# Kernel optimization log

Measured on AMD Instinct MI355X. Metric: run time of the kernel, lower is better.

Reference implementation:

```python
import jax, jax.numpy as jnp
import numpy as np

EPS = 1e-6
CONV_P = 3.0
GM_P = 2.0
NUM_NODES = 50000
NUM_EDGES = 600000
NUM_GRAPHS = 512
IN_DIM = 128
HID = 128
OUT_DIM = 64


def _scatter_mean(vals, index, num_segments):
    # scatter_mean with empty segments -> 0 (count clamped to 1)
    s = jax.ops.segment_sum(vals, index, num_segments=num_segments)
    cnt = jax.ops.segment_sum(jnp.ones((vals.shape[0],), vals.dtype), index,
                              num_segments=num_segments)
    return s / jnp.maximum(cnt, 1.0)[:, None]


def _signed_pow(v, p):
    return jnp.sign(v) * (jnp.abs(v) + EPS) ** p


def _spm_conv(x, W, b, src, dst, p):
    h = x @ W.T + b                      # [N, hid] linear
    msg = h[src]                          # gather x_j  [E, hid]
    t = _signed_pow(msg, p)
    pooled = _scatter_mean(t, dst, NUM_NODES)
    return _signed_pow(pooled, 1.0 / p)


def setup_inputs() -> dict:
    key = jax.random.key(0)
    ks = jax.random.split(key, 8)
    x = jax.random.normal(ks[0], (NUM_NODES, IN_DIM), jnp.float32)
    edge_index = jax.random.randint(ks[1], (2, NUM_EDGES), 0, NUM_NODES)
    batch = jnp.sort(jax.random.randint(ks[2], (NUM_NODES,), 0, NUM_GRAPHS))
    s1 = 1.0 / np.sqrt(IN_DIM)
    s2 = 1.0 / np.sqrt(HID)
    W1 = jax.random.uniform(ks[3], (HID, IN_DIM), jnp.float32, -s1, s1)
    b1 = jax.random.uniform(ks[4], (HID,), jnp.float32, -s1, s1)
    W2 = jax.random.uniform(ks[5], (HID, HID), jnp.float32, -s2, s2)
    b2 = jax.random.uniform(ks[6], (HID,), jnp.float32, -s2, s2)
    # final layer: orthogonal-init frozen weight (out_dim=64, hid=128)
    A = jax.random.normal(ks[7], (HID, OUT_DIM), jnp.float32)
    Q, _ = jnp.linalg.qr(A)
    Wout = Q.T                            # [OUT_DIM, HID], orthonormal rows
    bout = jax.random.uniform(jax.random.fold_in(key, 9), (OUT_DIM,),
                              jnp.float32, -s2, s2)
    return {"x": x, "W1": W1, "b1": b1, "W2": W2, "b2": b2,
            "Wout": Wout, "bout": bout, "edge_index": edge_index,
            "batch": batch}


def reference(x, W1, b1, W2, b2, Wout, bout, edge_index, batch):
    src, dst = edge_index[0], edge_index[1]
    h = _spm_conv(x, W1, b1, src, dst, CONV_P)
    h = jax.nn.relu(h)                    # relu between conv layers only
    h = _spm_conv(h, W2, b2, src, dst, CONV_P)
    # global generalized mean pool (signed)
    t = _signed_pow(h, GM_P)
    pooled = _scatter_mean(t, batch, NUM_GRAPHS)
    graph_repr = _signed_pow(pooled, 1.0 / GM_P)   # [G, HID]
    return graph_repr @ Wout.T + bout              # [G, OUT_DIM]
```

## Files before the change

### kernel.cpp

```cpp
#include <hip/hip_runtime.h>
#include <hip/hip_bf16.h>
#include <math.h>

#define N_NODES 50000
#define N_EDGES 600000
#define N_GRAPHS 512
#define DIM 128
#define OUTD 64
#define EPSV 1e-6f
#define BSTRIDE 64
#define EBLK4 586
#define PREP_BLK 64

typedef __attribute__((ext_vector_type(8))) short bf16x8;
typedef __attribute__((ext_vector_type(4))) float f32x4;

__device__ __forceinline__ float sgn(float v) {
    return (v > 0.f) ? 1.f : ((v < 0.f) ? -1.f : 0.f);
}

__device__ __forceinline__ float cube_signed(float v) {
    float m = fabsf(v) + EPSV;
    return sgn(v) * m * m * m;
}

__device__ __forceinline__ float cbrt_pos(float m) {
    return exp2f(log2f(m) * (1.0f / 3.0f));
}

__device__ __forceinline__ unsigned short f2bf(float f) {
    unsigned u = __float_as_uint(f);
    unsigned r = (u + 0x7fff + ((u >> 16) & 1)) >> 16;
    return (unsigned short)r;
}

__device__ __forceinline__ float bf2f(unsigned short h) {
    return __uint_as_float(((unsigned)h) << 16);
}

__device__ __forceinline__ void gather_acc8(const unsigned* __restrict__ T32,
                                            const unsigned short* __restrict__ bucket,
                                            int cnt, int lane, float2 acc[4]) {
    #pragma unroll
    for (int j = 0; j < 4; j++) acc[j] = make_float2(0.f, 0.f);
    if (cnt <= 0) return;
    int myidx = (lane < cnt) ? (int)bucket[lane] : 0;
    int sub = lane & 15, grp = lane >> 4;
    int cnt16 = (cnt + 15) & ~15;
    for (int i = 0; i < cnt16; i += 16) {
        uint4 u[4];
        #pragma unroll
        for (int c = 0; c < 4; c++) {
            int s = __shfl(myidx, i + c * 4 + grp, 64);
            u[c] = *(const uint4*)(T32 + (size_t)s * 64 + sub * 4);
        }
        #pragma unroll
        for (int c = 0; c < 4; c++) {
            acc[0].x += __uint_as_float(u[c].x << 16);
            acc[0].y += __uint_as_float(u[c].x & 0xffff0000u);
            acc[1].x += __uint_as_float(u[c].y << 16);
            acc[1].y += __uint_as_float(u[c].y & 0xffff0000u);
            acc[2].x += __uint_as_float(u[c].z << 16);
            acc[2].y += __uint_as_float(u[c].z & 0xffff0000u);
            acc[3].x += __uint_as_float(u[c].w << 16);
            acc[3].y += __uint_as_float(u[c].w & 0xffff0000u);
        }
    }
    #pragma unroll
    for (int j = 0; j < 4; j++) {
        acc[j].x += __shfl_xor(acc[j].x, 16, 64);
        acc[j].y += __shfl_xor(acc[j].y, 16, 64);
        acc[j].x += __shfl_xor(acc[j].x, 32, 64);
        acc[j].y += __shfl_xor(acc[j].y, 32, 64);
    }
}

__device__ __forceinline__ float acc_pick_x(const float2 acc[4], int grp) {
    return grp == 0 ? acc[0].x : grp == 1 ? acc[1].x : grp == 2 ? acc[2].x : acc[3].x;
}
__device__ __forceinline__ float acc_pick_y(const float2 acc[4], int grp) {
    return grp == 0 ? acc[0].y : grp == 1 ? acc[1].y : grp == 2 ? acc[2].y : acc[3].y;
}


__global__ void buildprep(const int* __restrict__ src, const int* __restrict__ dst,
                          int* __restrict__ deg, unsigned short* __restrict__ csr,
                          const float* __restrict__ W1, const float* __restrict__ W2,
                          unsigned short* __restrict__ W1hi, unsigned short* __restrict__ W1lo,
                          unsigned short* __restrict__ W2hi, unsigned short* __restrict__ W2lo,
                          const int* __restrict__ batch, int* __restrict__ gstart,
                          unsigned* __restrict__ T1z, unsigned* __restrict__ T2z) {
    int b = blockIdx.x;
    if (b < EBLK4) {
        int e4 = b * 256 + threadIdx.x;
        if (e4 < N_EDGES / 4) {
            uint4 s4 = ((const uint4*)src)[e4];
            uint4 d4 = ((const uint4*)dst)[e4];
            int d0 = (int)d4.x, d1 = (int)d4.y, d2 = (int)d4.z, d3 = (int)d4.w;
            int sl0 = atomicAdd(&deg[d0], 1);
            int sl1 = atomicAdd(&deg[d1], 1);
            int sl2 = atomicAdd(&deg[d2], 1);
            int sl3 = atomicAdd(&deg[d3], 1);
            if (sl0 < BSTRIDE) csr[d0 * BSTRIDE + sl0] = (unsigned short)(s4.x + 1);
            if (sl1 < BSTRIDE) csr[d1 * BSTRIDE + sl1] = (unsigned short)(s4.y + 1);
            if (sl2 < BSTRIDE) csr[d2 * BSTRIDE + sl2] = (unsigned short)(s4.z + 1);
            if (sl3 < BSTRIDE) csr[d3 * BSTRIDE + sl3] = (unsigned short)(s4.w + 1);
        }
        return;
    }
    int i = (b - EBLK4) * 256 + threadIdx.x;
    {
        float w = W1[i];
        unsigned short h = f2bf(w);
        W1hi[i] = h;
        W1lo[i] = f2bf(w - bf2f(h));
        w = W2[i];
        h = f2bf(w);
        W2hi[i] = h;
        W2lo[i] = f2bf(w - bf2f(h));
    }
    if (i < 64) { T1z[i] = 0u; T2z[i] = 0u; }
    if (i <= N_GRAPHS) {
        int lo = 0, hi = N_NODES;
        while (lo < hi) {
            int mid = (lo + hi) >> 1;
            if (batch[mid] < i) lo = mid + 1; else hi = mid;
        }
        gstart[i] = lo;
    }
}


__global__ __launch_bounds__(256) void linear_cube_mfma(const float* __restrict__ X,
                                                        const unsigned short* __restrict__ Whi,
                                                        const unsigned short* __restrict__ Wlo,
                                                        const float* __restrict__ B,
                                                        unsigned short* __restrict__ T) {
    __shared__ unsigned short Tl[4][16][DIM];
    int wave = threadIdx.x >> 6;
    int lane = threadIdx.x & 63;
    int tile = blockIdx.x * 4 + wave;
    if (tile >= N_NODES / 16) return;
    int n0 = tile * 16;
    int r = lane & 15;
    int g = lane >> 4;

    bf16x8 xh[4], xl[4];
    const float* xrow = X + (size_t)(n0 + r) * DIM + g * 8;
    #pragma unroll
    for (int kb = 0; kb < 4; kb++) {
        float4 a = *(const float4*)(xrow + kb * 32);
        float4 b = *(const float4*)(xrow + kb * 32 + 4);
        float v[8] = {a.x, a.y, a.z, a.w, b.x, b.y, b.z, b.w};
        #pragma unroll
        for (int j = 0; j < 8; j++) {
            unsigned short h = f2bf(v[j]);
            float rem = v[j] - bf2f(h);
            xh[kb][j] = (short)h;
            xl[kb][j] = (short)f2bf(rem);
        }
    }

    #pragma unroll
    for (int ct = 0; ct < 8; ct++) {
        const unsigned short* whbase = Whi + (size_t)(ct * 16 + r) * DIM + g * 8;
        const unsigned short* wlbase = Wlo + (size_t)(ct * 16 + r) * DIM + g * 8;
        f32x4 acc = {0.f, 0.f, 0.f, 0.f};
        #pragma unroll
        for (int kb = 0; kb < 4; kb++) {
            bf16x8 wh = *(const bf16x8*)(whbase + kb * 32);
            bf16x8 wl = *(const bf16x8*)(wlbase + kb * 32);
            acc = __builtin_amdgcn_mfma_f32_16x16x32_bf16(xh[kb], wh, acc, 0, 0, 0);
            acc = __builtin_amdgcn_mfma_f32_16x16x32_bf16(xl[kb], wh, acc, 0, 0, 0);
            acc = __builtin_amdgcn_mfma_f32_16x16x32_bf16(xh[kb], wl, acc, 0, 0, 0);
        }
        float bias = B[ct * 16 + r];
        #pragma unroll
        for (int q = 0; q < 4; q++) {
            int node = g * 4 + q;
            float h = acc[q] + bias;
            Tl[wave][node][ct * 16 + r] = f2bf(cube_signed(h));
        }
    }

    uint4* dstg = (uint4*)(T + (size_t)(n0 + 1) * DIM);
    const uint4* srcl = (const uint4*)&Tl[wave][0][0];
    #pragma unroll
    for (int i = 0; i < 4; i++) {
        dstg[i * 64 + lane] = srcl[i * 64 + lane];
    }
}


__global__ __launch_bounds__(512) void agg_linear_cube(const unsigned* __restrict__ T32,
                                                       const int* __restrict__ deg,
                                                       const unsigned short* __restrict__ csr,
                                                       const unsigned short* __restrict__ Whi,
                                                       const unsigned short* __restrict__ Wlo,
                                                       const float* __restrict__ B,
                                                       unsigned short* __restrict__ Tout) {
    __shared__ __attribute__((aligned(16))) unsigned Phi[16][68];
    __shared__ __attribute__((aligned(16))) unsigned Plo[16][68];
    int wave = threadIdx.x >> 6;
    int lane = threadIdx.x & 63;
    int n0 = blockIdx.x * 16;
    int sub = lane & 15, grp = lane >> 4;

    #pragma unroll
    for (int q = 0; q < 2; q++) {
        int row = wave * 2 + q;
        int nd = n0 + row;
        int d = deg[nd];
        int cnt = d < BSTRIDE ? d : BSTRIDE;
        float2 acc[4];
        gather_acc8(T32, csr + (size_t)nd * BSTRIDE, cnt, lane, acc);
        float c = (float)(d > 1 ? d : 1);
        float m0 = acc_pick_x(acc, grp) / c;
        float m1 = acc_pick_y(acc, grp) / c;
        float r0 = fmaxf(sgn(m0) * cbrt_pos(fabsf(m0) + EPSV), 0.f);
        float r1 = fmaxf(sgn(m1) * cbrt_pos(fabsf(m1) + EPSV), 0.f);
        unsigned short h0 = f2bf(r0), h1 = f2bf(r1);
        unsigned short l0 = f2bf(r0 - bf2f(h0)), l1 = f2bf(r1 - bf2f(h1));
        Phi[row][sub * 4 + grp] = (unsigned)h0 | ((unsigned)h1 << 16);
        Plo[row][sub * 4 + grp] = (unsigned)l0 | ((unsigned)l1 << 16);
    }
    __syncthreads();

    int r = lane & 15;
    int g = lane >> 4;
    bf16x8 xh[4], xl[4];
    #pragma unroll
    for (int kb = 0; kb < 4; kb++) {
        xh[kb] = *(const bf16x8*)&Phi[r][kb * 16 + g * 4];
        xl[kb] = *(const bf16x8*)&Plo[r][kb * 16 + g * 4];
    }
    int ct = wave;
    const unsigned short* whbase = Whi + (size_t)(ct * 16 + r) * DIM + g * 8;
    const unsigned short* wlbase = Wlo + (size_t)(ct * 16 + r) * DIM + g * 8;
    f32x4 acc = {0.f, 0.f, 0.f, 0.f};
    #pragma unroll
    for (int kb = 0; kb < 4; kb++) {
        bf16x8 wh = *(const bf16x8*)(whbase + kb * 32);
        bf16x8 wl = *(const bf16x8*)(wlbase + kb * 32);
        acc = __builtin_amdgcn_mfma_f32_16x16x32_bf16(xh[kb], wh, acc, 0, 0, 0);
        acc = __builtin_amdgcn_mfma_f32_16x16x32_bf16(xl[kb], wh, acc, 0, 0, 0);
        acc = __builtin_amdgcn_mfma_f32_16x16x32_bf16(xh[kb], wl, acc, 0, 0, 0);
    }
    float bias = B[ct * 16 + r];
    #pragma unroll
    for (int q = 0; q < 4; q++) {
        int node = g * 4 + q;
        float h = acc[q] + bias;
        Tout[(size_t)(n0 + node + 1) * DIM + ct * 16 + r] = f2bf(cube_signed(h));
    }
}


__global__ __launch_bounds__(256) void aggregate(const unsigned* __restrict__ T32,
                                                 const int* __restrict__ deg,
                                                 const unsigned short* __restrict__ csr,
                                                 float* __restrict__ P) {
    int nd = blockIdx.x * 4 + (threadIdx.x >> 6);
    if (nd >= N_NODES) return;
    int lane = threadIdx.x & 63;
    int sub = lane & 15, grp = lane >> 4;
    int d = deg[nd];
    int cnt = d < BSTRIDE ? d : BSTRIDE;
    float2 acc[4];
    gather_acc8(T32, csr + (size_t)nd * BSTRIDE, cnt, lane, acc);
    float c = (float)(d > 1 ? d : 1);
    float m0 = acc_pick_x(acc, grp) / c;
    float m1 = acc_pick_y(acc, grp) / c;
    float r0 = sgn(m0) * cbrt_pos(fabsf(m0) + EPSV);
    float r1 = sgn(m1) * cbrt_pos(fabsf(m1) + EPSV);
    *(float2*)(P + (size_t)nd * DIM + sub * 8 + grp * 2) = make_float2(r0, r1);
}


__global__ __launch_bounds__(128) void pool_final(const float* __restrict__ P,
                                                  const int* __restrict__ gstart,
                                                  const float* __restrict__ Wout,
                                                  const float* __restrict__ bout,
                                                  float* __restrict__ out) {
    __shared__ float R[DIM];
    __shared__ float partial[128];
    int g = blockIdx.x, f = threadIdx.x;
    int s = gstart[g], e = gstart[g + 1];
    float acc = 0.f;
    for (int i = s; i < e; i++) {
        float v = P[(size_t)i * DIM + f];
        float m = fabsf(v) + EPSV;
        acc += sgn(v) * m * m;
    }
    int cnt = e - s;
    float c = (float)(cnt > 1 ? cnt : 1);
    float mean = acc / c;
    R[f] = sgn(mean) * sqrtf(fabsf(mean) + EPSV);
    __syncthreads();

    int o = f & 63;
    int half = f >> 6;
    const float4* W4 = (const float4*)Wout + o * 32 + half * 16;
    const float4* R4 = (const float4*)R + half * 16;
    float a = 0.f;
    #pragma unroll
    for (int k = 0; k < 16; k++) {
        float4 w = W4[k];
        float4 r = R4[k];
        a += r.x * w.x + r.y * w.y + r.z * w.z + r.w * w.w;
    }
    partial[f] = a;
    __syncthreads();
    if (f < OUTD) out[(size_t)g * OUTD + f] = bout[f] + partial[f] + partial[f + 64];
}


extern "C" void kernel_launch(void* const* d_in, const int* in_sizes, int n_in,
                              void* d_out, int out_size, void* d_ws, size_t ws_size,
                              hipStream_t stream) {
    const float* x    = (const float*)d_in[0];
    const float* W1   = (const float*)d_in[1];
    const float* b1   = (const float*)d_in[2];
    const float* W2   = (const float*)d_in[3];
    const float* b2   = (const float*)d_in[4];
    const float* Wout = (const float*)d_in[5];
    const float* bout = (const float*)d_in[6];
    const int* edge   = (const int*)d_in[7];
    const int* batch  = (const int*)d_in[8];
    const int* srcp = edge;
    const int* dstp = edge + N_EDGES;
    float* out = (float*)d_out;

    char* ws = (char*)d_ws;
    size_t off = 0;
    auto alloc = [&](size_t bytes) -> char* {
        char* p = ws + off;
        off += (bytes + 255) / 256 * 256;
        return p;
    };
    unsigned short* T1 = (unsigned short*)alloc((size_t)(N_NODES + 1) * DIM * 2);
    unsigned short* T2 = (unsigned short*)alloc((size_t)(N_NODES + 1) * DIM * 2);
    float* P        = (float*)alloc((size_t)N_NODES * DIM * 4);
    int*   deg      = (int*)alloc((size_t)N_NODES * 4);
    unsigned short* csr = (unsigned short*)alloc((size_t)N_NODES * BSTRIDE * 2);
    int*   gstart   = (int*)alloc((size_t)(N_GRAPHS + 1) * 4);
    unsigned short* W1hi = (unsigned short*)alloc((size_t)DIM * DIM * 2);
    unsigned short* W1lo = (unsigned short*)alloc((size_t)DIM * DIM * 2);
    unsigned short* W2hi = (unsigned short*)alloc((size_t)DIM * DIM * 2);
    unsigned short* W2lo = (unsigned short*)alloc((size_t)DIM * DIM * 2);

    hipMemsetAsync(deg, 0, (size_t)N_NODES * 4, stream);
    buildprep<<<EBLK4 + PREP_BLK, 256, 0, stream>>>(srcp, dstp, deg, csr,
                                                    W1, W2, W1hi, W1lo, W2hi, W2lo,
                                                    batch, gstart,
                                                    (unsigned*)T1, (unsigned*)T2);

    const int TILES = N_NODES / 16;
    const int LBLK = (TILES + 3) / 4;
    const int ABLK = (N_NODES + 3) / 4;
    linear_cube_mfma<<<LBLK, 256, 0, stream>>>(x, W1hi, W1lo, b1, T1);
    agg_linear_cube<<<TILES, 512, 0, stream>>>((const unsigned*)T1, deg, csr,
                                               W2hi, W2lo, b2, T2);
    aggregate<<<ABLK, 256, 0, stream>>>((const unsigned*)T2, deg, csr, P);
    pool_final<<<N_GRAPHS, 128, 0, stream>>>(P, gstart, Wout, bout, out);
}
```

Baseline: 182.9 us.

## Split neighbor aggregation into feature-sliced passes and unfuse second linear layer

Replaces the fused aggregate+linear kernel and the separate aggregate kernel with one feature-sliced gather kernel run in four passes over 32-column slices. Each pass touches one quarter of the node feature table, so the gathered working set is more likely to stay in L2 cache across random neighbor accesses. The second linear layer becomes a standalone MFMA kernel reading hi/lo bf16 splits from global buffers. This costs four times the index loads and shuffles, extra global round-trips for the intermediate, and an added launch.

Result: slower. 388.7 us (+112.6%).

```diff
diff --git a/kernel.cpp b/kernel.cpp
--- a/kernel.cpp
+++ b/kernel.cpp
@@ -11,9 +11,11 @@
 #define BSTRIDE 64
 #define EBLK4 586
 #define PREP_BLK 64
+#define NGRP 12500
 
 typedef __attribute__((ext_vector_type(8))) short bf16x8;
 typedef __attribute__((ext_vector_type(4))) float f32x4;
+typedef __attribute__((ext_vector_type(4))) unsigned u32x4;
 
 __device__ __forceinline__ float sgn(float v) {
     return (v > 0.f) ? 1.f : ((v < 0.f) ? -1.f : 0.f);
@@ -36,50 +38,6 @@
 
 __device__ __forceinline__ float bf2f(unsigned short h) {
     return __uint_as_float(((unsigned)h) << 16);
-}
-
-__device__ __forceinline__ void gather_acc8(const unsigned* __restrict__ T32,
-                                            const unsigned short* __restrict__ bucket,
-                                            int cnt, int lane, float2 acc[4]) {
-    #pragma unroll
-    for (int j = 0; j < 4; j++) acc[j] = make_float2(0.f, 0.f);
-    if (cnt <= 0) return;
-    int myidx = (lane < cnt) ? (int)bucket[lane] : 0;
-    int sub = lane & 15, grp = lane >> 4;
-    int cnt16 = (cnt + 15) & ~15;
-    for (int i = 0; i < cnt16; i += 16) {
-        uint4 u[4];
-        #pragma unroll
-        for (int c = 0; c < 4; c++) {
-            int s = __shfl(myidx, i + c * 4 + grp, 64);
-            u[c] = *(const uint4*)(T32 + (size_t)s * 64 + sub * 4);
-        }
-        #pragma unroll
-        for (int c = 0; c < 4; c++) {
-            acc[0].x += __uint_as_float(u[c].x << 16);
-            acc[0].y += __uint_as_float(u[c].x & 0xffff0000u);
-            acc[1].x += __uint_as_float(u[c].y << 16);
-            acc[1].y += __uint_as_float(u[c].y & 0xffff0000u);
-            acc[2].x += __uint_as_float(u[c].z << 16);
-            acc[2].y += __uint_as_float(u[c].z & 0xffff0000u);
-            acc[3].x += __uint_as_float(u[c].w << 16);
-            acc[3].y += __uint_as_float(u[c].w & 0xffff0000u);
-        }
-    }
-    #pragma unroll
-    for (int j = 0; j < 4; j++) {
-        acc[j].x += __shfl_xor(acc[j].x, 16, 64);
-        acc[j].y += __shfl_xor(acc[j].y, 16, 64);
-        acc[j].x += __shfl_xor(acc[j].x, 32, 64);
-        acc[j].y += __shfl_xor(acc[j].y, 32, 64);
-    }
-}
-
-__device__ __forceinline__ float acc_pick_x(const float2 acc[4], int grp) {
-    return grp == 0 ? acc[0].x : grp == 1 ? acc[1].x : grp == 2 ? acc[2].x : acc[3].x;
-}
-__device__ __forceinline__ float acc_pick_y(const float2 acc[4], int grp) {
-    return grp == 0 ? acc[0].y : grp == 1 ? acc[1].y : grp == 2 ? acc[2].y : acc[3].y;
 }
 
 
@@ -192,88 +150,136 @@
 }
 
 
-__global__ __launch_bounds__(512) void agg_linear_cube(const unsigned* __restrict__ T32,
-                                                       const int* __restrict__ deg,
-                                                       const unsigned short* __restrict__ csr,
-                                                       const unsigned short* __restrict__ Whi,
-                                                       const unsigned short* __restrict__ Wlo,
-                                                       const float* __restrict__ B,
-                                                       unsigned short* __restrict__ Tout) {
-    __shared__ __attribute__((aligned(16))) unsigned Phi[16][68];
-    __shared__ __attribute__((aligned(16))) unsigned Plo[16][68];
+__global__ __launch_bounds__(256) void agg_sliced(const unsigned* __restrict__ T32,
+                                                  const int* __restrict__ deg,
+                                                  const unsigned short* __restrict__ csr,
+                                                  unsigned* __restrict__ Phi,
+                                                  unsigned* __restrict__ Plo,
+                                                  float* __restrict__ P, int mode) {
+    int bid = blockIdx.x;
+    int pass = bid / NGRP;
+    int grp = bid - pass * NGRP;
     int wave = threadIdx.x >> 6;
     int lane = threadIdx.x & 63;
-    int n0 = blockIdx.x * 16;
-    int sub = lane & 15, grp = lane >> 4;
-
-    #pragma unroll
-    for (int q = 0; q < 2; q++) {
-        int row = wave * 2 + q;
-        int nd = n0 + row;
-        int d = deg[nd];
-        int cnt = d < BSTRIDE ? d : BSTRIDE;
-        float2 acc[4];
-        gather_acc8(T32, csr + (size_t)nd * BSTRIDE, cnt, lane, acc);
+    int nd = grp * 4 + wave;
+    int es = lane >> 2, q = lane & 3;
+
+    int d = deg[nd];
+    int cnt = d < BSTRIDE ? d : BSTRIDE;
+    const unsigned short* bucket = csr + (size_t)nd * BSTRIDE;
+    int myidx = (lane < cnt) ? (int)__builtin_nontemporal_load(&bucket[lane]) : 0;
+
+    float a[8];
+    #pragma unroll
+    for (int j = 0; j < 8; j++) a[j] = 0.f;
+
+    for (int i = 0; i < cnt; i += 16) {
+        int s = __shfl(myidx, i + es, 64);
+        u32x4 u = *(const u32x4*)(T32 + (size_t)s * 64 + pass * 16 + q * 4);
+        a[0] += __uint_as_float(u.x << 16);
+        a[1] += __uint_as_float(u.x & 0xffff0000u);
+        a[2] += __uint_as_float(u.y << 16);
+        a[3] += __uint_as_float(u.y & 0xffff0000u);
+        a[4] += __uint_as_float(u.z << 16);
+        a[5] += __uint_as_float(u.z & 0xffff0000u);
+        a[6] += __uint_as_float(u.w << 16);
+        a[7] += __uint_as_float(u.w & 0xffff0000u);
+    }
+    #pragma unroll
+    for (int j = 0; j < 8; j++) {
+        a[j] += __shfl_xor(a[j], 4, 64);
+        a[j] += __shfl_xor(a[j], 8, 64);
+        a[j] += __shfl_xor(a[j], 16, 64);
+        a[j] += __shfl_xor(a[j], 32, 64);
+    }
+
+    if (es == 0) {
         float c = (float)(d > 1 ? d : 1);
-        float m0 = acc_pick_x(acc, grp) / c;
-        float m1 = acc_pick_y(acc, grp) / c;
-        float r0 = fmaxf(sgn(m0) * cbrt_pos(fabsf(m0) + EPSV), 0.f);
-        float r1 = fmaxf(sgn(m1) * cbrt_pos(fabsf(m1) + EPSV), 0.f);
-        unsigned short h0 = f2bf(r0), h1 = f2bf(r1);
-        unsigned short l0 = f2bf(r0 - bf2f(h0)), l1 = f2bf(r1 - bf2f(h1));
-        Phi[row][sub * 4 + grp] = (unsigned)h0 | ((unsigned)h1 << 16);
-        Plo[row][sub * 4 + grp] = (unsigned)l0 | ((unsigned)l1 << 16);
-    }
-    __syncthreads();
-
+        float r[8];
+        #pragma unroll
+        for (int j = 0; j < 8; j++) {
+            float m = a[j] / c;
+            float v = sgn(m) * cbrt_pos(fabsf(m) + EPSV);
+            r[j] = (mode == 0) ? fmaxf(v, 0.f) : v;
+        }
+        if (mode == 0) {
+            u32x4 hw, lw;
+            unsigned short h0, h1;
+            h0 = f2bf(r[0]); h1 = f2bf(r[1]);
+            hw.x = (unsigned)h0 | ((unsigned)h1 << 16);
+            lw.x = (unsigned)f2bf(r[0] - bf2f(h0)) | ((unsigned)f2bf(r[1] - bf2f(h1)) << 16);
+            h0 = f2bf(r[2]); h1 = f2bf(r[3]);
+            hw.y = (unsigned)h0 | ((unsigned)h1 << 16);
+            lw.y = (unsigned)f2bf(r[2] - bf2f(h0)) | ((unsigned)f2bf(r[3] - bf2f(h1)) << 16);
+            h0 = f2bf(r[4]); h1 = f2bf(r[5]);
+            hw.z = (unsigned)h0 | ((unsigned)h1 << 16);
+            lw.z = (unsigned)f2bf(r[4] - bf2f(h0)) | ((unsigned)f2bf(r[5] - bf2f(h1)) << 16);
+            h0 = f2bf(r[6]); h1 = f2bf(r[7]);
+            hw.w = (unsigned)h0 | ((unsigned)h1 << 16);
+            lw.w = (unsigned)f2bf(r[6] - bf2f(h0)) | ((unsigned)f2bf(r[7] - bf2f(h1)) << 16);
+            __builtin_nontemporal_store(hw, (u32x4*)(Phi + (size_t)nd * 64 + pass * 16 + q * 4));
+            __builtin_nontemporal_store(lw, (u32x4*)(Plo + (size_t)nd * 64 + pass * 16 + q * 4));
+        } else {
+            f32x4 w0 = {r[0], r[1], r[2], r[3]};
+            f32x4 w1 = {r[4], r[5], r[6], r[7]};
+            float* dst = P + (size_t)nd * DIM + pass * 32 + q * 8;
+            __builtin_nontemporal_store(w0, (f32x4*)dst);
+            __builtin_nontemporal_store(w1, (f32x4*)(dst + 4));
+        }
+    }
+}
+
+
+__global__ __launch_bounds__(256) void lin2_mfma(const unsigned* __restrict__ Phi,
+                                                 const unsigned* __restrict__ Plo,
+                                                 const unsigned short* __restrict__ Whi,
+                                                 const unsigned short* __restrict__ Wlo,
+                                                 const float* __restrict__ B,
+                                                 unsigned short* __restrict__ T) {
+    __shared__ unsigned short Tl[4][16][DIM];
+    int wave = threadIdx.x >> 6;
+    int lane = threadIdx.x & 63;
+    int tile = blockIdx.x * 4 + wave;
+    if (tile >= N_NODES / 16) return;
+    int n0 = tile * 16;
     int r = lane & 15;
     int g = lane >> 4;
+
     bf16x8 xh[4], xl[4];
     #pragma unroll
     for (int kb = 0; kb < 4; kb++) {
-        xh[kb] = *(const bf16x8*)&Phi[r][kb * 16 + g * 4];
-        xl[kb] = *(const bf16x8*)&Plo[r][kb * 16 + g * 4];
-    }
-    int ct = wave;
-    const unsigned short* whbase = Whi + (size_t)(ct * 16 + r) * DIM + g * 8;
-    const unsigned short* wlbase = Wlo + (size_t)(ct * 16 + r) * DIM + g * 8;
-    f32x4 acc = {0.f, 0.f, 0.f, 0.f};
-    #pragma unroll
-    for (int kb = 0; kb < 4; kb++) {
-        bf16x8 wh = *(const bf16x8*)(whbase + kb * 32);
-        bf16x8 wl = *(const bf16x8*)(wlbase + kb * 32);
-        acc = __builtin_amdgcn_mfma_f32_16x16x32_bf16(xh[kb], wh, acc, 0, 0, 0);
-        acc = __builtin_amdgcn_mfma_f32_16x16x32_bf16(xl[kb], wh, acc, 0, 0, 0);
-        acc = __builtin_amdgcn_mfma_f32_16x16x32_bf16(xh[kb], wl, acc, 0, 0, 0);
-    }
-    float bias = B[ct * 16 + r];
-    #pragma unroll
-    for (int q = 0; q < 4; q++) {
-        int node = g * 4 + q;
-        float h = acc[q] + bias;
-        Tout[(size_t)(n0 + node + 1) * DIM + ct * 16 + r] = f2bf(cube_signed(h));
-    }
-}
-
-
-__global__ __launch_bounds__(256) void aggregate(const unsigned* __restrict__ T32,
-                                                 const int* __restrict__ deg,
-                                                 const unsigned short* __restrict__ csr,
-                                                 float* __restrict__ P) {
-    int nd = blockIdx.x * 4 + (threadIdx.x >> 6);
-    if (nd >= N_NODES) return;
-    int lane = threadIdx.x & 63;
-    int sub = lane & 15, grp = lane >> 4;
-    int d = deg[nd];
-    int cnt = d < BSTRIDE ? d : BSTRIDE;
-    float2 acc[4];
-    gather_acc8(T32, csr + (size_t)nd * BSTRIDE, cnt, lane, acc);
-    float c = (float)(d > 1 ? d : 1);
-    float m0 = acc_pick_x(acc, grp) / c;
-    float m1 = acc_pick_y(acc, grp) / c;
-    float r0 = sgn(m0) * cbrt_pos(fabsf(m0) + EPSV);
-    float r1 = sgn(m1) * cbrt_pos(fabsf(m1) + EPSV);
-    *(float2*)(P + (size_t)nd * DIM + sub * 8 + grp * 2) = make_float2(r0, r1);
+        xh[kb] = *(const bf16x8*)(Phi + (size_t)(n0 + r) * 64 + kb * 16 + g * 4);
+        xl[kb] = *(const bf16x8*)(Plo + (size_t)(n0 + r) * 64 + kb * 16 + g * 4);
+    }
+
+    #pragma unroll
+    for (int ct = 0; ct < 8; ct++) {
+        const unsigned short* whbase = Whi + (size_t)(ct * 16 + r) * DIM + g * 8;
+        const unsigned short* wlbase = Wlo + (size_t)(ct * 16 + r) * DIM + g * 8;
+        f32x4 acc = {0.f, 0.f, 0.f, 0.f};
+        #pragma unroll
+        for (int kb = 0; kb < 4; kb++) {
+            bf16x8 wh = *(const bf16x8*)(whbase + kb * 32);
+            bf16x8 wl = *(const bf16x8*)(wlbase + kb * 32);
+            acc = __builtin_amdgcn_mfma_f32_16x16x32_bf16(xh[kb], wh, acc, 0, 0, 0);
+            acc = __builtin_amdgcn_mfma_f32_16x16x32_bf16(xl[kb], wh, acc, 0, 0, 0);
+            acc = __builtin_amdgcn_mfma_f32_16x16x32_bf16(xh[kb], wl, acc, 0, 0, 0);
+        }
+        float bias = B[ct * 16 + r];
+        #pragma unroll
+        for (int q = 0; q < 4; q++) {
+            int node = g * 4 + q;
+            float h = acc[q] + bias;
+            Tl[wave][node][ct * 16 + r] = f2bf(cube_signed(h));
+        }
+    }
+
+    uint4* dstg = (uint4*)(T + (size_t)(n0 + 1) * DIM);
+    const uint4* srcl = (const uint4*)&Tl[wave][0][0];
+    #pragma unroll
+    for (int i = 0; i < 4; i++) {
+        dstg[i * 64 + lane] = srcl[i * 64 + lane];
+    }
 }
 
 
@@ -341,6 +347,8 @@
     unsigned short* T1 = (unsigned short*)alloc((size_t)(N_NODES + 1) * DIM * 2);
     unsigned short* T2 = (unsigned short*)alloc((size_t)(N_NODES + 1) * DIM * 2);
     float* P        = (float*)alloc((size_t)N_NODES * DIM * 4);
+    unsigned* Phi   = (unsigned*)alloc((size_t)N_NODES * 64 * 4);
+    unsigned* Plo   = (unsigned*)alloc((size_t)N_NODES * 64 * 4);
     int*   deg      = (int*)alloc((size_t)N_NODES * 4);
     unsigned short* csr = (unsigned short*)alloc((size_t)N_NODES * BSTRIDE * 2);
     int*   gstart   = (int*)alloc((size_t)(N_GRAPHS + 1) * 4);
@@ -357,10 +365,11 @@
 
     const int TILES = N_NODES / 16;
     const int LBLK = (TILES + 3) / 4;
-    const int ABLK = (N_NODES + 3) / 4;
     linear_cube_mfma<<<LBLK, 256, 0, stream>>>(x, W1hi, W1lo, b1, T1);
-    agg_linear_cube<<<TILES, 512, 0, stream>>>((const unsigned*)T1, deg, csr,
-                                               W2hi, W2lo, b2, T2);
-    aggregate<<<ABLK, 256, 0, stream>>>((const unsigned*)T2, deg, csr, P);
+    agg_sliced<<<4 * NGRP, 256, 0, stream>>>((const unsigned*)T1, deg, csr,
+                                             Phi, Plo, P, 0);
+    lin2_mfma<<<LBLK, 256, 0, stream>>>(Phi, Plo, W2hi, W2lo, b2, T2);
+    agg_sliced<<<4 * NGRP, 256, 0, stream>>>((const unsigned*)T2, deg, csr,
+                                             Phi, Plo, P, 1);
     pool_final<<<N_GRAPHS, 128, 0, stream>>>(P, gstart, Wout, bout, out);
 }
```
